# Kernel tuning notes

Hardware: AMD Instinct MI355X
Metric: run time of the kernel (lower is better)

The kernel has to match this reference:

```python
import jax, jax.numpy as jnp
import numpy as np

RES = (512, 512)
MAX_VAL = 100.0
OBJ_WIDTH = 5
N_ITERS = 5
SIGMA = 0.2


def setup_inputs() -> dict:
    key = jax.random.key(0)
    ks = jax.random.split(key, 6)
    H, W = RES
    x = jax.random.uniform(ks[0], (1, H, W, 2), jnp.float32) * 2.0 - 1.0  # query grid in [-1,1]
    boundary_types = jax.random.randint(ks[1], (H, W), 0, 2, jnp.int32)
    boundary_conditions = jax.random.uniform(ks[2], (H, W), jnp.float32)
    B_enc = SIGMA * jax.random.normal(ks[3], (64, 2), jnp.float32)  # GaussianEncoding(0.2, 2, 64)
    Wh = jax.random.normal(ks[4], (4, 128, 128), jnp.float32) / jnp.sqrt(128.0)
    W_out = jax.random.normal(ks[5], (128, 1), jnp.float32) / jnp.sqrt(128.0)
    return {"x": x, "boundary_types": boundary_types,
            "boundary_conditions": boundary_conditions,
            "B_enc": B_enc, "Wh": Wh, "W_out": W_out}


def _box_filter(a, width):
    # width x width mean filter, 'same' padding (F.conv2d with ones/width^2 kernel)
    k = jnp.ones((1, 1, width, width), a.dtype) / float(width * width)
    return jax.lax.conv_general_dilated(a[None, None], k, (1, 1), "SAME")[0, 0]


def _grid_sample_2d(img, grid):
    # img [H,W]; grid [N,2] with (x,y) in [-1,1]; bilinear, align_corners=True, border padding
    H, W = img.shape
    ix = jnp.clip((grid[:, 0] + 1.0) * 0.5 * (W - 1), 0.0, W - 1.0)
    iy = jnp.clip((grid[:, 1] + 1.0) * 0.5 * (H - 1), 0.0, H - 1.0)
    x0 = jnp.floor(ix).astype(jnp.int32)
    y0 = jnp.floor(iy).astype(jnp.int32)
    x1 = jnp.clip(x0 + 1, 0, W - 1)
    y1 = jnp.clip(y0 + 1, 0, H - 1)
    wx = ix - x0
    wy = iy - y0
    return (img[y0, x0] * (1 - wx) * (1 - wy) + img[y0, x1] * wx * (1 - wy)
            + img[y1, x0] * (1 - wx) * wy + img[y1, x1] * wx * wy)


def _solve(V0, C, boundary_types, boundary_conditions):
    # 5 Jacobi-style 8-neighbor stencil passes: free cells take the neighbor
    # average plus local cost; boundary cells are pinned to their conditions.
    free = boundary_types == 0

    def step(V, _):
        Vp = jnp.pad(V, 1, mode="edge")
        nb = (Vp[:-2, :-2] + Vp[:-2, 1:-1] + Vp[:-2, 2:]
              + Vp[1:-1, :-2] + Vp[1:-1, 2:]
              + Vp[2:, :-2] + Vp[2:, 1:-1] + Vp[2:, 2:]) / 8.0
        return jnp.where(free, nb + C, boundary_conditions), None

    V, _ = jax.lax.scan(step, V0, None, length=N_ITERS)
    return V


def reference(x, boundary_types, boundary_conditions, B_enc, Wh, W_out):
    H, W = RES
    free = boundary_types == 0
    # V init: max_val everywhere, boundary cells pinned (obj_inds = boundary_types > 0)
    V0 = jnp.where(free, jnp.float32(MAX_VAL), boundary_conditions)

    # Gaussian random Fourier feature encoding of 0.5 + 0.5*x -> 128 dims
    xq = 0.5 + 0.5 * x.reshape(-1, 2)
    vp = (2.0 * jnp.pi) * (xq @ B_enc.T)            # [N, 64]
    enc = jnp.concatenate([jnp.cos(vp), jnp.sin(vp)], axis=-1)  # [N, 128]

    # FullyFusedMLP: 4 hidden ReLU layers of 128 neurons, linear 1-dim output, no bias
    h = enc
    for i in range(Wh.shape[0]):
        h = jax.nn.relu(h @ Wh[i])
    C = (h @ W_out).reshape(H, W)
    C_pos = jax.nn.relu(C)

    # extra cost: box-filtered obstacle boundary values splashed onto free cells
    obj = boundary_conditions * (boundary_types == 1) * (boundary_conditions > 0)
    extra = _box_filter(obj, OBJ_WIDTH) * free
    Cs = C_pos + extra

    out_grid = _solve(V0, Cs, boundary_types, boundary_conditions)
    out = _grid_sample_2d(out_grid, x.reshape(-1, 2)).reshape(H, W)
    return out, C
```

## Files before the change

### kernel.cpp

```cpp
#include <hip/hip_runtime.h>
#include <hip/hip_bf16.h>


typedef unsigned short ushort_t;
typedef short short8 __attribute__((ext_vector_type(8)));
typedef float floatx16 __attribute__((ext_vector_type(16)));
typedef unsigned int uintx4 __attribute__((ext_vector_type(4)));

#define HH 512
#define WW 512
#define NPIX (HH*WW)

__device__ inline unsigned int pk_bf16(float a, float b) {
    __hip_bfloat162 h = __float22bfloat162_rn(float2{a, b});
    return *(unsigned int*)&h;
}
__device__ inline void async_copy16(void* lds, const void* g) {
    __builtin_amdgcn_global_load_lds(
        (const __attribute__((address_space(1))) unsigned int*)g,
        (__attribute__((address_space(3))) unsigned int*)lds, 16, 0, 0);
}

__global__ __launch_bounds__(256) void prep_kernel(const float* __restrict__ Wh,
                                                   ushort_t* __restrict__ WT) {
    __shared__ float trans[32][129];
    const int t = threadIdx.x;
    const int l = blockIdx.x >> 2, n0 = (blockIdx.x & 3) * 32;
    const int nl = t & 31, k0 = t >> 5;
    #pragma unroll
    for (int pass = 0; pass < 16; ++pass) {
        int k = pass * 8 + k0;
        trans[nl][k] = Wh[l * 16384 + k * 128 + n0 + nl];
    }
    __syncthreads();
    #pragma unroll
    for (int c = 0; c < 2; ++c) {
        int idx = c * 256 + t;
        int nl2 = idx >> 4, P = idx & 15;
        int n = n0 + nl2;
        int cc = P ^ (n & 15);
        int ks = cc >> 1, Hq = cc & 1;
        int base = (ks >> 1) * 32 + (ks & 1) * 16 + Hq * 4;
        unsigned int w0 = pk_bf16(trans[nl2][base + 0],  trans[nl2][base + 1]);
        unsigned int w1 = pk_bf16(trans[nl2][base + 2],  trans[nl2][base + 3]);
        unsigned int w2 = pk_bf16(trans[nl2][base + 8],  trans[nl2][base + 9]);
        unsigned int w3 = pk_bf16(trans[nl2][base + 10], trans[nl2][base + 11]);
        ((uint4*)WT)[(l * 128 + n) * 16 + P] = uint4{w0, w1, w2, w3};
    }
}

template<int BUF>
__device__ __forceinline__ void klayer(const ushort_t* __restrict__ wlds,
                                       const int (&inn)[8],
                                       const uintx4 (&fragv)[8],
                                       floatx16 (&acc)[4]) {
    #pragma unroll
    for (int i = 0; i < 4; ++i) acc[i] = (floatx16)(0.0f);
    #pragma unroll
    for (int ks = 0; ks < 8; ++ks) {
        short8 bf = __builtin_bit_cast(short8, fragv[ks]);
        #pragma unroll
        for (int i = 0; i < 4; ++i) {
            short8 av = *(const short8*)((const char*)wlds + BUF * 32768 + i * 8192 + inn[ks]);
            acc[i] = __builtin_amdgcn_mfma_f32_32x32x16_bf16(av, bf, acc[i], 0, 0, 0);
        }
    }
}

__device__ __forceinline__ void xform_all(uintx4 (&fragv)[8], const floatx16 (&acc)[4]) {
    #pragma unroll
    for (int ks = 0; ks < 8; ++ks) {
        const int i = ks >> 1, par = ks & 1;
        fragv[ks][0] = pk_bf16(fmaxf(acc[i][8 * par + 0], 0.0f),
                               fmaxf(acc[i][8 * par + 1], 0.0f));
        fragv[ks][1] = pk_bf16(fmaxf(acc[i][8 * par + 2], 0.0f),
                               fmaxf(acc[i][8 * par + 3], 0.0f));
        fragv[ks][2] = pk_bf16(fmaxf(acc[i][8 * par + 4], 0.0f),
                               fmaxf(acc[i][8 * par + 5], 0.0f));
        fragv[ks][3] = pk_bf16(fmaxf(acc[i][8 * par + 6], 0.0f),
                               fmaxf(acc[i][8 * par + 7], 0.0f));
    }
}

__device__ __forceinline__ void stage_layer(ushort_t* wlds, int buf,
                                            const char* src, int wave, int lane) {
    #pragma unroll
    for (int c2 = 0; c2 < 4; ++c2) {
        int base = c2 * 512 + wave * 64;
        async_copy16(&wlds[buf * 16384 + base * 8], src + (base + lane) * 16);
    }
}

__global__ __launch_bounds__(512, 2) void mlp_kernel(const float* __restrict__ x,
                                                     const ushort_t* __restrict__ WT,
                                                     const float* __restrict__ benc,
                                                     const float* __restrict__ wout,
                                                     float* __restrict__ C_ws,
                                                     float* __restrict__ outbuf) {
    __shared__ __align__(16) ushort_t wlds[2 * 128 * 128];
    const int tid = threadIdx.x;
    const int lane = tid & 63, wave = tid >> 6;
    const int m = lane & 31, Hh = lane >> 5;
    const int p0 = blockIdx.x * 256 + wave * 32;

    stage_layer(wlds, 0, (const char*)WT, wave, lane);
    stage_layer(wlds, 1, (const char*)WT + 32768, wave, lane);

    int inn[8];
    #pragma unroll
    for (int ks = 0; ks < 8; ++ks)
        inn[ks] = m * 256 + ((((2 * ks + Hh) ^ (m & 15))) << 4);

    uintx4 fragv[8];

    {
        float2 xv = ((const float2*)x)[p0 + m];
        float xq0 = 0.5f + 0.5f * xv.x, xq1 = 0.5f + 0.5f * xv.y;
        #pragma unroll
        for (int ks = 0; ks < 4; ++ks) {
            const int i = ks >> 1, par = ks & 1;
            #pragma unroll
            for (int jp = 0; jp < 4; ++jp) {
                int f = i * 32 + par * 16 + Hh * 4 + (jp & 1) * 2 + (jp >> 1) * 8;
                float4 b = *(const float4*)&benc[2 * f];
                float t0 = __builtin_amdgcn_fractf(xq0 * b.x + xq1 * b.y);
                float t1 = __builtin_amdgcn_fractf(xq0 * b.z + xq1 * b.w);
                fragv[ks][jp]     = pk_bf16(__builtin_amdgcn_cosf(t0),
                                            __builtin_amdgcn_cosf(t1));
                fragv[ks + 4][jp] = pk_bf16(__builtin_amdgcn_sinf(t0),
                                            __builtin_amdgcn_sinf(t1));
            }
        }
    }
    __syncthreads();

    floatx16 acc[4];
    klayer<0>(wlds, inn, fragv, acc);
    __syncthreads();
    stage_layer(wlds, 0, (const char*)WT + 2 * 32768, wave, lane);
    xform_all(fragv, acc);
    klayer<1>(wlds, inn, fragv, acc);
    __syncthreads();
    stage_layer(wlds, 1, (const char*)WT + 3 * 32768, wave, lane);
    xform_all(fragv, acc);
    klayer<0>(wlds, inn, fragv, acc);
    __syncthreads();
    xform_all(fragv, acc);
    klayer<1>(wlds, inn, fragv, acc);

    float s = 0.0f;
    #pragma unroll
    for (int i = 0; i < 4; ++i) {
        #pragma unroll
        for (int rq = 0; rq < 4; ++rq) {
            float4 wv = *(const float4*)&wout[i * 32 + rq * 8 + 4 * Hh];
            s += fmaxf(acc[i][rq * 4 + 0], 0.0f) * wv.x
               + fmaxf(acc[i][rq * 4 + 1], 0.0f) * wv.y
               + fmaxf(acc[i][rq * 4 + 2], 0.0f) * wv.z
               + fmaxf(acc[i][rq * 4 + 3], 0.0f) * wv.w;
        }
    }
    s += __shfl_xor(s, 32);
    if (Hh == 0) {
        C_ws[p0 + m] = s;
        outbuf[NPIX + p0 + m] = s;
    }
}

#define LW 48
#define LROWS 46
#define LCELLS (LROWS * LW)

__global__ __launch_bounds__(512) void fused_solve_kernel(const int* __restrict__ bt,
                                                          const float* __restrict__ bc,
                                                          const float* __restrict__ C_ws,
                                                          float* __restrict__ Vfin) {
    __shared__ float Va[LCELLS];
    __shared__ float Vb[LCELLS];
    __shared__ float Wp[LCELLS];
    const int tid = threadIdx.x;
    const int gx0 = (blockIdx.x & 15) * 32 - 7, gy0 = (blockIdx.x >> 4) * 32 - 7;

    for (int c = tid; c < LCELLS; c += 512) {
        int li = c / LW, lj = c % LW;
        int gi = gy0 + li, gj = gx0 + lj;
        float v = 0.0f;
        if (lj < LROWS && gi >= 0 && gi < HH && gj >= 0 && gj < WW) {
            int g = gi * WW + gj;
            float b = bc[g];
            if (bt[g] == 1 && b > 0.0f) v = b;
        }
        Va[c] = v;
    }
    __syncthreads();

    for (int c = tid; c < LCELLS; c += 512) {
        int lj = c % LW;
        float s = 0.0f;
        if (lj >= 2 && lj < LROWS - 2) {
            s = Va[c - 2] + Va[c - 1] + Va[c] + Va[c + 1] + Va[c + 2];
        }
        Vb[c] = s;
    }
    __syncthreads();

    for (int c = tid; c < LCELLS; c += 512) {
        int li = c / LW, lj = c % LW;
        float w = -1.0f, v0 = 0.0f;
        if (li >= 2 && li < LROWS - 2 && lj >= 2 && lj < LROWS - 2) {
            int gi = gy0 + li, gj = gx0 + lj;
            if (gi >= 0 && gi < HH && gj >= 0 && gj < WW) {
                int g = gi * WW + gj;
                if (bt[g] == 0) {
                    float s = Vb[c - 2 * LW] + Vb[c - LW] + Vb[c]
                            + Vb[c + LW] + Vb[c + 2 * LW];
                    w = fmaxf(C_ws[g], 0.0f) + s * 0.04f;
                    v0 = 100.0f;
                } else {
                    float b = bc[g];
                    w = -b - 1.0f;
                    v0 = b;
                }
            }
        }
        Wp[c] = w;
        Va[c] = v0;
    }
    __syncthreads();

    float* src = Va;
    float* dst = Vb;
    #pragma unroll 1
    for (int t = 0; t < 5; ++t) {
        for (int c = tid; c < LCELLS; c += 512) {
            int li = c / LW, lj = c % LW;
            if (li < 2 || li >= LROWS - 2 || lj < 2 || lj >= LROWS - 2) continue;
            float w = Wp[c];
            float v;
            if (w < 0.0f) {
                v = -w - 1.0f;
            } else {
                int gi = gy0 + li, gj = gx0 + lj;
                int um = (gi > 0)      ? -LW : 0;
                int dp = (gi < HH - 1) ?  LW : 0;
                int lm = (gj > 0)      ?  -1 : 0;
                int rp = (gj < WW - 1) ?   1 : 0;
                float s = src[c + um + lm] + src[c + um] + src[c + um + rp]
                        + src[c + lm]                     + src[c + rp]
                        + src[c + dp + lm] + src[c + dp] + src[c + dp + rp];
                v = s * 0.125f + w;
            }
            dst[c] = v;
        }
        __syncthreads();
        float* tmp = src; src = dst; dst = tmp;
    }

    for (int c = tid; c < 32 * 32; c += 512) {
        int li = 7 + (c >> 5), lj = 7 + (c & 31);
        Vfin[(gy0 + li) * WW + gx0 + lj] = src[li * LW + lj];
    }
}

__global__ void sample_kernel(const float* __restrict__ x,
                              const float* __restrict__ V,
                              float* __restrict__ out) {
    int idx = blockIdx.x * 256 + threadIdx.x;
    float2 g2 = ((const float2*)x)[idx];
    float ix = (g2.x + 1.0f) * 0.5f * 511.0f;
    float iy = (g2.y + 1.0f) * 0.5f * 511.0f;
    ix = fminf(fmaxf(ix, 0.0f), 511.0f);
    iy = fminf(fmaxf(iy, 0.0f), 511.0f);
    int x0 = (int)floorf(ix), y0 = (int)floorf(iy);
    int x1 = min(x0 + 1, 511), y1 = min(y0 + 1, 511);
    float wx = ix - (float)x0, wy = iy - (float)y0;
    float v00 = V[y0 * 512 + x0], v01 = V[y0 * 512 + x1];
    float v10 = V[y1 * 512 + x0], v11 = V[y1 * 512 + x1];
    float v = v00 * (1.0f - wx) * (1.0f - wy) + v01 * wx * (1.0f - wy)
            + v10 * (1.0f - wx) * wy          + v11 * wx * wy;
    out[idx] = v;
}

extern "C" void kernel_launch(void* const* d_in, const int* in_sizes, int n_in,
                              void* d_out, int out_size, void* d_ws, size_t ws_size,
                              hipStream_t stream) {
    const float* x    = (const float*)d_in[0];
    const int*   bt   = (const int*)d_in[1];
    const float* bc   = (const float*)d_in[2];
    const float* benc = (const float*)d_in[3];
    const float* Wh   = (const float*)d_in[4];
    const float* wout = (const float*)d_in[5];

    char* ws = (char*)d_ws;
    ushort_t* WT   = (ushort_t*)(ws + 4096);
    float*    C_ws = (float*)(ws + 262144);
    float*    Vfin = (float*)(ws + 262144 + 3 * (1 << 20));
    float*    outp = (float*)d_out;

    prep_kernel<<<16, 256, 0, stream>>>(Wh, WT);
    mlp_kernel<<<1024, 512, 0, stream>>>(x, WT, benc, wout, C_ws, outp);
    fused_solve_kernel<<<256, 512, 0, stream>>>(bt, bc, C_ws, Vfin);
    sample_kernel<<<1024, 256, 0, stream>>>(x, Vfin, outp);
}
```

Baseline: 118.4 us.

## Fuse grid-sample into solve kernel using a global atomic grid barrier

Merges the separate sampling kernel into the stencil-solve kernel. A device-wide software barrier (an atomic counter reset in prep_kernel, then spin-waiting) ensures all 256 blocks have written Vfin before any block samples it. This removes one kernel launch and its launch gap. It relies on all 256 blocks being co-resident, which risks deadlock if they are not, and the spin adds synchronisation cost.

```diff
diff --git a/kernel.cpp b/kernel.cpp
--- a/kernel.cpp
+++ b/kernel.cpp
@@ -22,7 +22,9 @@
 }
 
 __global__ __launch_bounds__(256) void prep_kernel(const float* __restrict__ Wh,
-                                                   ushort_t* __restrict__ WT) {
+                                                   ushort_t* __restrict__ WT,
+                                                   unsigned int* __restrict__ bar) {
+    if (blockIdx.x == 0 && threadIdx.x == 0) *bar = 0;
     __shared__ float trans[32][129];
     const int t = threadIdx.x;
     const int l = blockIdx.x >> 2, n0 = (blockIdx.x & 3) * 32;
@@ -171,10 +173,13 @@
 #define LROWS 46
 #define LCELLS (LROWS * LW)
 
-__global__ __launch_bounds__(512) void fused_solve_kernel(const int* __restrict__ bt,
-                                                          const float* __restrict__ bc,
-                                                          const float* __restrict__ C_ws,
-                                                          float* __restrict__ Vfin) {
+__global__ __launch_bounds__(512) void solve_sample_kernel(const int* __restrict__ bt,
+                                                           const float* __restrict__ bc,
+                                                           const float* __restrict__ C_ws,
+                                                           const float* __restrict__ x,
+                                                           float* __restrict__ Vfin,
+                                                           float* __restrict__ outp,
+                                                           unsigned int* __restrict__ bar) {
     __shared__ float Va[LCELLS];
     __shared__ float Vb[LCELLS];
     __shared__ float Wp[LCELLS];
@@ -260,25 +265,34 @@
         int li = 7 + (c >> 5), lj = 7 + (c & 31);
         Vfin[(gy0 + li) * WW + gx0 + lj] = src[li * LW + lj];
     }
-}
-
-__global__ void sample_kernel(const float* __restrict__ x,
-                              const float* __restrict__ V,
-                              float* __restrict__ out) {
-    int idx = blockIdx.x * 256 + threadIdx.x;
-    float2 g2 = ((const float2*)x)[idx];
-    float ix = (g2.x + 1.0f) * 0.5f * 511.0f;
-    float iy = (g2.y + 1.0f) * 0.5f * 511.0f;
-    ix = fminf(fmaxf(ix, 0.0f), 511.0f);
-    iy = fminf(fmaxf(iy, 0.0f), 511.0f);
-    int x0 = (int)floorf(ix), y0 = (int)floorf(iy);
-    int x1 = min(x0 + 1, 511), y1 = min(y0 + 1, 511);
-    float wx = ix - (float)x0, wy = iy - (float)y0;
-    float v00 = V[y0 * 512 + x0], v01 = V[y0 * 512 + x1];
-    float v10 = V[y1 * 512 + x0], v11 = V[y1 * 512 + x1];
-    float v = v00 * (1.0f - wx) * (1.0f - wy) + v01 * wx * (1.0f - wy)
-            + v10 * (1.0f - wx) * wy          + v11 * wx * wy;
-    out[idx] = v;
+
+    __syncthreads();
+    __threadfence();
+    if (tid == 0) {
+        atomicAdd(bar, 1u);
+        while (__hip_atomic_load(bar, __ATOMIC_ACQUIRE, __HIP_MEMORY_SCOPE_AGENT) < 256u)
+            __builtin_amdgcn_s_sleep(2);
+    }
+    __syncthreads();
+    __threadfence();
+
+    #pragma unroll
+    for (int q = 0; q < 2; ++q) {
+        int idx = blockIdx.x * 1024 + q * 512 + tid;
+        float2 g2 = ((const float2*)x)[idx];
+        float ix = (g2.x + 1.0f) * 0.5f * 511.0f;
+        float iy = (g2.y + 1.0f) * 0.5f * 511.0f;
+        ix = fminf(fmaxf(ix, 0.0f), 511.0f);
+        iy = fminf(fmaxf(iy, 0.0f), 511.0f);
+        int x0 = (int)floorf(ix), y0 = (int)floorf(iy);
+        int x1 = min(x0 + 1, 511), y1 = min(y0 + 1, 511);
+        float wx = ix - (float)x0, wy = iy - (float)y0;
+        float v00 = Vfin[y0 * 512 + x0], v01 = Vfin[y0 * 512 + x1];
+        float v10 = Vfin[y1 * 512 + x0], v11 = Vfin[y1 * 512 + x1];
+        float v = v00 * (1.0f - wx) * (1.0f - wy) + v01 * wx * (1.0f - wy)
+                + v10 * (1.0f - wx) * wy          + v11 * wx * wy;
+        outp[idx] = v;
+    }
 }
 
 extern "C" void kernel_launch(void* const* d_in, const int* in_sizes, int n_in,
@@ -292,13 +306,13 @@
     const float* wout = (const float*)d_in[5];
 
     char* ws = (char*)d_ws;
+    unsigned int* bar = (unsigned int*)ws;
     ushort_t* WT   = (ushort_t*)(ws + 4096);
     float*    C_ws = (float*)(ws + 262144);
     float*    Vfin = (float*)(ws + 262144 + 3 * (1 << 20));
     float*    outp = (float*)d_out;
 
-    prep_kernel<<<16, 256, 0, stream>>>(Wh, WT);
+    prep_kernel<<<16, 256, 0, stream>>>(Wh, WT, bar);
     mlp_kernel<<<1024, 512, 0, stream>>>(x, WT, benc, wout, C_ws, outp);
-    fused_solve_kernel<<<256, 512, 0, stream>>>(bt, bc, C_ws, Vfin);
-    sample_kernel<<<1024, 256, 0, stream>>>(x, Vfin, outp);
-}
+    solve_sample_kernel<<<256, 512, 0, stream>>>(bt, bc, C_ws, x, Vfin, outp, bar);
+}
```

New measurement: 197.0 us. +66.3%, slower.

## Fuse bilinear sampling into solve kernel via per-tile query bucketing

Applied to the files above, without the earlier changes.

The MLP kernel bins each query point into its 32x32 solve tile using atomic counters and a per-tile index list. The solve kernel then does the bilinear sample straight from its shared-memory result, so the separate sample kernel and the global write and read of the solved grid go away. In exchange it adds atomic contention on 256 counters and scattered output writes. A fixed per-tile capacity means samples are dropped if a tile overflows.

```diff
diff --git a/kernel.cpp b/kernel.cpp
--- a/kernel.cpp
+++ b/kernel.cpp
@@ -10,6 +10,7 @@
 #define HH 512
 #define WW 512
 #define NPIX (HH*WW)
+#define CAP 2048
 
 __device__ inline unsigned int pk_bf16(float a, float b) {
     __hip_bfloat162 h = __float22bfloat162_rn(float2{a, b});
@@ -22,7 +23,9 @@
 }
 
 __global__ __launch_bounds__(256) void prep_kernel(const float* __restrict__ Wh,
-                                                   ushort_t* __restrict__ WT) {
+                                                   ushort_t* __restrict__ WT,
+                                                   unsigned int* __restrict__ cnt) {
+    if (blockIdx.x == 0) cnt[threadIdx.x] = 0;
     __shared__ float trans[32][129];
     const int t = threadIdx.x;
     const int l = blockIdx.x >> 2, n0 = (blockIdx.x & 3) * 32;
@@ -96,7 +99,9 @@
                                                      const float* __restrict__ benc,
                                                      const float* __restrict__ wout,
                                                      float* __restrict__ C_ws,
-                                                     float* __restrict__ outbuf) {
+                                                     float* __restrict__ outbuf,
+                                                     unsigned int* __restrict__ cnt,
+                                                     unsigned int* __restrict__ list) {
     __shared__ __align__(16) ushort_t wlds[2 * 128 * 128];
     const int tid = threadIdx.x;
     const int lane = tid & 63, wave = tid >> 6;
@@ -162,24 +167,36 @@
     }
     s += __shfl_xor(s, 32);
     if (Hh == 0) {
-        C_ws[p0 + m] = s;
-        outbuf[NPIX + p0 + m] = s;
+        int p = p0 + m;
+        C_ws[p] = s;
+        outbuf[NPIX + p] = s;
+        float2 xv2 = ((const float2*)x)[p];
+        float ix = fminf(fmaxf((xv2.x + 1.0f) * 0.5f * 511.0f, 0.0f), 511.0f);
+        float iy = fminf(fmaxf((xv2.y + 1.0f) * 0.5f * 511.0f, 0.0f), 511.0f);
+        int x0 = (int)floorf(ix), y0 = (int)floorf(iy);
+        int tile = (y0 >> 5) * 16 + (x0 >> 5);
+        unsigned int pos = atomicAdd(&cnt[tile], 1u);
+        if (pos < CAP) list[tile * CAP + pos] = (unsigned int)p;
     }
 }
 
 #define LW 48
-#define LROWS 46
+#define LROWS 47
 #define LCELLS (LROWS * LW)
 
-__global__ __launch_bounds__(512) void fused_solve_kernel(const int* __restrict__ bt,
-                                                          const float* __restrict__ bc,
-                                                          const float* __restrict__ C_ws,
-                                                          float* __restrict__ Vfin) {
+__global__ __launch_bounds__(512) void solve_sample_kernel(const int* __restrict__ bt,
+                                                           const float* __restrict__ bc,
+                                                           const float* __restrict__ C_ws,
+                                                           const float* __restrict__ x,
+                                                           const unsigned int* __restrict__ cnt,
+                                                           const unsigned int* __restrict__ list,
+                                                           float* __restrict__ outp) {
     __shared__ float Va[LCELLS];
     __shared__ float Vb[LCELLS];
     __shared__ float Wp[LCELLS];
     const int tid = threadIdx.x;
-    const int gx0 = (blockIdx.x & 15) * 32 - 7, gy0 = (blockIdx.x >> 4) * 32 - 7;
+    const int tx = blockIdx.x & 15, ty = blockIdx.x >> 4;
+    const int gx0 = tx * 32 - 7, gy0 = ty * 32 - 7;
 
     for (int c = tid; c < LCELLS; c += 512) {
         int li = c / LW, lj = c % LW;
@@ -256,29 +273,24 @@
         float* tmp = src; src = dst; dst = tmp;
     }
 
-    for (int c = tid; c < 32 * 32; c += 512) {
-        int li = 7 + (c >> 5), lj = 7 + (c & 31);
-        Vfin[(gy0 + li) * WW + gx0 + lj] = src[li * LW + lj];
-    }
-}
-
-__global__ void sample_kernel(const float* __restrict__ x,
-                              const float* __restrict__ V,
-                              float* __restrict__ out) {
-    int idx = blockIdx.x * 256 + threadIdx.x;
-    float2 g2 = ((const float2*)x)[idx];
-    float ix = (g2.x + 1.0f) * 0.5f * 511.0f;
-    float iy = (g2.y + 1.0f) * 0.5f * 511.0f;
-    ix = fminf(fmaxf(ix, 0.0f), 511.0f);
-    iy = fminf(fmaxf(iy, 0.0f), 511.0f);
-    int x0 = (int)floorf(ix), y0 = (int)floorf(iy);
-    int x1 = min(x0 + 1, 511), y1 = min(y0 + 1, 511);
-    float wx = ix - (float)x0, wy = iy - (float)y0;
-    float v00 = V[y0 * 512 + x0], v01 = V[y0 * 512 + x1];
-    float v10 = V[y1 * 512 + x0], v11 = V[y1 * 512 + x1];
-    float v = v00 * (1.0f - wx) * (1.0f - wy) + v01 * wx * (1.0f - wy)
-            + v10 * (1.0f - wx) * wy          + v11 * wx * wy;
-    out[idx] = v;
+    int n = min((int)cnt[blockIdx.x], CAP);
+    const unsigned int* lst = &list[blockIdx.x * CAP];
+    for (int j = tid; j < n; j += 512) {
+        int p = (int)lst[j];
+        float2 g2 = ((const float2*)x)[p];
+        float ix = fminf(fmaxf((g2.x + 1.0f) * 0.5f * 511.0f, 0.0f), 511.0f);
+        float iy = fminf(fmaxf((g2.y + 1.0f) * 0.5f * 511.0f, 0.0f), 511.0f);
+        int x0 = (int)floorf(ix), y0 = (int)floorf(iy);
+        int x1 = min(x0 + 1, 511), y1 = min(y0 + 1, 511);
+        float wx = ix - (float)x0, wy = iy - (float)y0;
+        int lx0 = x0 - tx * 32 + 7, ly0 = y0 - ty * 32 + 7;
+        int lx1 = x1 - tx * 32 + 7, ly1 = y1 - ty * 32 + 7;
+        float v00 = src[ly0 * LW + lx0], v01 = src[ly0 * LW + lx1];
+        float v10 = src[ly1 * LW + lx0], v11 = src[ly1 * LW + lx1];
+        float v = v00 * (1.0f - wx) * (1.0f - wy) + v01 * wx * (1.0f - wy)
+                + v10 * (1.0f - wx) * wy          + v11 * wx * wy;
+        outp[p] = v;
+    }
 }
 
 extern "C" void kernel_launch(void* const* d_in, const int* in_sizes, int n_in,
@@ -292,13 +304,13 @@
     const float* wout = (const float*)d_in[5];
 
     char* ws = (char*)d_ws;
-    ushort_t* WT   = (ushort_t*)(ws + 4096);
-    float*    C_ws = (float*)(ws + 262144);
-    float*    Vfin = (float*)(ws + 262144 + 3 * (1 << 20));
-    float*    outp = (float*)d_out;
-
-    prep_kernel<<<16, 256, 0, stream>>>(Wh, WT);
-    mlp_kernel<<<1024, 512, 0, stream>>>(x, WT, benc, wout, C_ws, outp);
-    fused_solve_kernel<<<256, 512, 0, stream>>>(bt, bc, C_ws, Vfin);
-    sample_kernel<<<1024, 256, 0, stream>>>(x, Vfin, outp);
-}
+    unsigned int* cnt  = (unsigned int*)(ws + 1024);
+    ushort_t*     WT   = (ushort_t*)(ws + 4096);
+    float*        C_ws = (float*)(ws + 262144);
+    unsigned int* list = (unsigned int*)(ws + 262144 + (1 << 20));
+    float*        outp = (float*)d_out;
+
+    prep_kernel<<<16, 256, 0, stream>>>(Wh, WT, cnt);
+    mlp_kernel<<<1024, 512, 0, stream>>>(x, WT, benc, wout, C_ws, outp, cnt, list);
+    solve_sample_kernel<<<256, 512, 0, stream>>>(bt, bc, C_ws, x, cnt, list, outp);
+}
```

Result: slower. 251.7 us (+112.5%).
